# Kernel tuning notes

Hardware: AMD Instinct MI355X
Metric: run time of the kernel (lower is better)

Reference implementation:

```python
import jax, jax.numpy as jnp
import numpy as np

N = 100000      # nodes (single node type)
E = 400000      # edges per relation
R = 4           # relations
DIN = 128       # h_dim
H1 = 8          # heads, layer 1
DH1 = DIN // H1 # per-head dim, layer 1
DOUT = 128      # out_dim (layer 2 has 1 head of dim DOUT)
NEG_SLOPE = 0.2 # GATConv default leaky_relu slope


def gat_rel_layer(h, src, dst, W, al, ar, loop_w, bias, activation):
    """One RelationalAttLayer: per-relation GATConv (bias=False), summed across
    relations, + self-loop matmul + bias + optional relu. dropout=0.
    h: [N, din]; src/dst: [R, E]; W: [R, din, H*Dh]; al/ar: [R, H, Dh];
    loop_w: [din, dout]; bias: [dout]."""
    n = h.shape[0]

    def per_rel(src_r, dst_r, W_r, al_r, ar_r):
        nh, dh = al_r.shape
        Wh = (h @ W_r).reshape(n, nh, dh)                 # [N,H,Dh]
        el = jnp.sum(Wh * al_r, axis=-1)                  # [N,H]
        er = jnp.sum(Wh * ar_r, axis=-1)                  # [N,H]
        e = jax.nn.leaky_relu(el[src_r] + er[dst_r], NEG_SLOPE)  # [E,H]
        # edge-softmax over incoming edges per destination node (stable)
        m = jax.lax.stop_gradient(jax.ops.segment_max(e, dst_r, num_segments=n))
        ex = jnp.exp(e - m[dst_r])
        denom = jax.ops.segment_sum(ex, dst_r, num_segments=n)  # [N,H]
        alpha = ex / denom[dst_r]                                # [E,H]
        # scatter-aggregate messages
        return jax.ops.segment_sum(alpha[:, :, None] * Wh[src_r], dst_r,
                                   num_segments=n)               # [N,H,Dh]

    outs = jax.vmap(per_rel)(src, dst, W, al, ar)  # [R,N,H,Dh]
    hout = outs.sum(0).reshape(n, -1)              # cross-relation sum, flatten heads
    hout = hout + h @ loop_w + bias                # self-loop + h_bias
    if activation:
        hout = jax.nn.relu(hout)
    return hout


def setup_inputs() -> dict:
    key = jax.random.key(0)
    ks = jax.random.split(key, 14)
    s = 0.1
    return {
        "h": jax.random.normal(ks[0], (N, DIN), dtype=jnp.float32),
        "src_idx": jax.random.randint(ks[1], (R, E), 0, N, dtype=jnp.int32),
        "dst_idx": jax.random.randint(ks[2], (R, E), 0, N, dtype=jnp.int32),
        # layer 1 params (h_dim -> h_dim, H1 heads)
        "W1": jax.random.normal(ks[3], (R, DIN, H1 * DH1), dtype=jnp.float32) * s,
        "al1": jax.random.normal(ks[4], (R, H1, DH1), dtype=jnp.float32) * s,
        "ar1": jax.random.normal(ks[5], (R, H1, DH1), dtype=jnp.float32) * s,
        "loop1": jax.random.normal(ks[6], (DIN, DIN), dtype=jnp.float32) * s,
        "b1": jnp.zeros((DIN,), dtype=jnp.float32),
        # layer 2 params (h_dim -> out_dim, 1 head)
        "W2": jax.random.normal(ks[7], (R, DIN, DOUT), dtype=jnp.float32) * s,
        "al2": jax.random.normal(ks[8], (R, 1, DOUT), dtype=jnp.float32) * s,
        "ar2": jax.random.normal(ks[9], (R, 1, DOUT), dtype=jnp.float32) * s,
        "loop2": jax.random.normal(ks[10], (DIN, DOUT), dtype=jnp.float32) * s,
        "b2": jnp.zeros((DOUT,), dtype=jnp.float32),
    }


def reference(h, src_idx, dst_idx, W1, al1, ar1, loop1, b1,
              W2, al2, ar2, loop2, b2):
    # hidden layer: relu activation; last layer: no activation (last_layer_act=False)
    h1 = gat_rel_layer(h, src_idx, dst_idx, W1, al1, ar1, loop1, b1, activation=True)
    h2 = gat_rel_layer(h1, src_idx, dst_idx, W2, al2, ar2, loop2, b2, activation=False)
    return h2
```

## Files before the change

kernel.cpp:

```cpp
#include <hip/hip_runtime.h>

#define NN 100000
#define NE 400000
#define NREL 4
#define MAXDEG 24

typedef unsigned short u16;
typedef __attribute__((ext_vector_type(8))) short bf16x8;
typedef __attribute__((ext_vector_type(4))) float f32x4;

__device__ __forceinline__ u16 f2bf(float x) {
    union { float f; unsigned int u; } v; v.f = x;
    unsigned int r = v.u + 0x7fffu + ((v.u >> 16) & 1u);
    return (u16)(r >> 16);
}
__device__ __forceinline__ float bf2f(u16 x) {
    union { unsigned int u; float f; } v; v.u = ((unsigned int)x) << 16;
    return v.f;
}

template <bool RELU>
__global__ __launch_bounds__(256) void conv_kernel(
    const float* __restrict__ X, u16* __restrict__ Xb, int n8)
{
    int i = blockIdx.x * 256 + threadIdx.x;
    if (i >= n8) return;
    float4 a = ((const float4*)X)[2 * i];
    float4 b = ((const float4*)X)[2 * i + 1];
    if (RELU) {
        a.x = fmaxf(a.x, 0.f); a.y = fmaxf(a.y, 0.f);
        a.z = fmaxf(a.z, 0.f); a.w = fmaxf(a.w, 0.f);
        b.x = fmaxf(b.x, 0.f); b.y = fmaxf(b.y, 0.f);
        b.z = fmaxf(b.z, 0.f); b.w = fmaxf(b.w, 0.f);
    }
    ushort4 lo, hi;
    lo.x = f2bf(a.x); lo.y = f2bf(a.y); lo.z = f2bf(a.z); lo.w = f2bf(a.w);
    hi.x = f2bf(b.x); hi.y = f2bf(b.y); hi.z = f2bf(b.z); hi.w = f2bf(b.w);
    ((ushort4*)Xb)[2 * i] = lo;
    ((ushort4*)Xb)[2 * i + 1] = hi;
}

__global__ __launch_bounds__(256) void build_b_kernel(
    const float* __restrict__ W, const float* __restrict__ loopw,
    u16* __restrict__ Bb)
{
    int id = blockIdx.x * 256 + threadIdx.x;
    if (id >= 5 * 16384) return;
    int j = id >> 14, rem = id & 16383;
    int c = rem >> 7, k = rem & 127;
    const float* M = (j < 4) ? (W + j * 16384) : loopw;
    Bb[id] = f2bf(M[k * 128 + c]);
}

__global__ __launch_bounds__(256) void build_w_kernel(
    const float* __restrict__ W, const float* __restrict__ al,
    const float* __restrict__ ar, u16* __restrict__ wcatB, int nh, int dh)
{
    int id = blockIdx.x * 256 + threadIdx.x;
    if (id >= 16384) return;
    int j = id >> 7, k = id & 127;
    int P2 = 8 * nh;
    float s = 0.f;
    if (j < P2) {
        int half = 4 * nh;
        int jj = (j < half) ? j : j - half;
        const float* av = (j < half) ? al : ar;
        int r = jj / nh, h = jj % nh;
        for (int i = 0; i < dh; ++i)
            s += W[r * 16384 + k * 128 + h * dh + i] * av[(r * nh + h) * dh + i];
    }
    wcatB[j * 128 + k] = f2bf(s);
}

__global__ __launch_bounds__(256) void csr_build_kernel(
    const int* __restrict__ src, const int* __restrict__ dst,
    int* __restrict__ cur, int* __restrict__ bucket)
{
    int i = blockIdx.x * 256 + threadIdx.x;
    if (i >= NE) return;
    int d0 = dst[i],          s0 = src[i];
    int d1 = dst[NE + i],     s1 = src[NE + i];
    int d2 = dst[2 * NE + i], s2 = src[2 * NE + i];
    int d3 = dst[3 * NE + i], s3 = src[3 * NE + i];
    int p0 = atomicAdd(&cur[d0], 1);
    int p1 = atomicAdd(&cur[NN + d1], 1);
    int p2 = atomicAdd(&cur[2 * NN + d2], 1);
    int p3 = atomicAdd(&cur[3 * NN + d3], 1);
    if (p0 < MAXDEG) bucket[(size_t)d0 * MAXDEG + p0] = s0;
    if (p1 < MAXDEG) bucket[((size_t)NN + d1) * MAXDEG + p1] = s1;
    if (p2 < MAXDEG) bucket[((size_t)2 * NN + d2) * MAXDEG + p2] = s2;
    if (p3 < MAXDEG) bucket[((size_t)3 * NN + d3) * MAXDEG + p3] = s3;
}

__global__ __launch_bounds__(256) void fused_gemm_kernel(
    const u16* __restrict__ Xb, const u16* __restrict__ Bb,
    const u16* __restrict__ wcatB, u16* __restrict__ Wh,
    float* __restrict__ O, const float* __restrict__ bias,
    float* __restrict__ elr, int P2, int n)
{
    __shared__ u16 sA[64][136];
    __shared__ u16 sB[128][136];
    const int tid = threadIdx.x;
    const int y = blockIdx.y;
    const int row0 = blockIdx.x * 64;
    const u16* Bmat = (y < 5) ? (Bb + (size_t)y * 16384) : wcatB;

#pragma unroll
    for (int i = 0; i < 8; ++i) {
        int idx = tid + 256 * i;
        int r = idx >> 4, ch = idx & 15;
        *(float4*)&sB[r][ch * 8] = ((const float4*)Bmat)[idx];
    }
#pragma unroll
    for (int i = 0; i < 4; ++i) {
        int idx = tid + 256 * i;
        int r = idx >> 4, ch = idx & 15;
        int gr = row0 + r;
        float4 v = make_float4(0.f, 0.f, 0.f, 0.f);
        if (gr < n) v = *(const float4*)(Xb + (size_t)gr * 128 + ch * 8);
        *(float4*)&sA[r][ch * 8] = v;
    }
    __syncthreads();

    const int w = tid >> 6, lane = tid & 63;
    const int lr = lane & 15, hi = lane >> 4;
    f32x4 acc[8];
#pragma unroll
    for (int fn = 0; fn < 8; ++fn) acc[fn] = (f32x4){0.f, 0.f, 0.f, 0.f};
#pragma unroll
    for (int ko = 0; ko < 4; ++ko) {
        const int kk = ko * 32 + hi * 8;
        bf16x8 a = *(const bf16x8*)&sA[w * 16 + lr][kk];
#pragma unroll
        for (int fn = 0; fn < 8; ++fn) {
            bf16x8 b = *(const bf16x8*)&sB[fn * 16 + lr][kk];
            acc[fn] = __builtin_amdgcn_mfma_f32_16x16x32_bf16(a, b, acc[fn], 0, 0, 0);
        }
    }

    if (y < 4) {
        u16* Wr = Wh + (size_t)y * NN * 128;
#pragma unroll
        for (int reg = 0; reg < 4; ++reg) {
            int grow = row0 + w * 16 + hi * 4 + reg;
            if (grow >= n) continue;
            u16* crow = Wr + (size_t)grow * 128;
#pragma unroll
            for (int fn = 0; fn < 8; ++fn)
                crow[fn * 16 + lr] = f2bf(acc[fn][reg]);
        }
    } else if (y == 4) {
#pragma unroll
        for (int reg = 0; reg < 4; ++reg) {
            int grow = row0 + w * 16 + hi * 4 + reg;
            if (grow >= n) continue;
            float* crow = O + (size_t)grow * 128;
#pragma unroll
            for (int fn = 0; fn < 8; ++fn) {
                int col = fn * 16 + lr;
                crow[col] = acc[fn][reg] + bias[col];
            }
        }
    } else {
#pragma unroll
        for (int reg = 0; reg < 4; ++reg) {
            int grow = row0 + w * 16 + hi * 4 + reg;
            if (grow >= n) continue;
#pragma unroll
            for (int fn = 0; fn < 8; ++fn) {
                int col = fn * 16 + lr;
                if (col < P2) elr[(size_t)grow * P2 + col] = acc[fn][reg];
            }
        }
    }
}

__global__ __launch_bounds__(256) void gather_kernel(
    const int* __restrict__ cnt, const int* __restrict__ bucket,
    const float* __restrict__ elr, const u16* __restrict__ Wh,
    float* __restrict__ O, int ST, int nh, int dh_shift)
{
    const int d = blockIdx.x;
    const int w = threadIdx.x >> 6;
    const int lane = threadIdx.x & 63;
    const int c0 = lane * 2;
    const int hh = c0 >> dh_shift;
    __shared__ float2 part[4][64];

    float M0 = 0.f, M1 = 0.f;
    int deg = cnt[w * NN + d];
    deg = deg > MAXDEG ? MAXDEG : deg;
    if (deg > 0) {
        const int* bk = bucket + ((size_t)w * NN + d) * MAXDEG;
        const float erd = elr[(size_t)d * ST + NREL * nh + w * nh + hh];
        const u16* whr = Wh + (size_t)w * NN * 128;
        const int eo = w * nh + hh;
        float dn = 0.f, m0 = 0.f, m1 = 0.f;
        int e = 0;
        for (; e + 4 <= deg; e += 4) {
            int4 q = *(const int4*)(bk + e);
            float va = elr[(size_t)q.x * ST + eo];
            float vb = elr[(size_t)q.y * ST + eo];
            float vc = elr[(size_t)q.z * ST + eo];
            float vd = elr[(size_t)q.w * ST + eo];
            ushort2 wa = *(const ushort2*)(whr + (size_t)q.x * 128 + c0);
            ushort2 wb = *(const ushort2*)(whr + (size_t)q.y * 128 + c0);
            ushort2 wc = *(const ushort2*)(whr + (size_t)q.z * 128 + c0);
            ushort2 wd = *(const ushort2*)(whr + (size_t)q.w * 128 + c0);
            float v, ex;
            v = va + erd; v = v > 0.f ? v : 0.2f * v; ex = __expf(v);
            dn += ex; m0 = fmaf(ex, bf2f(wa.x), m0); m1 = fmaf(ex, bf2f(wa.y), m1);
            v = vb + erd; v = v > 0.f ? v : 0.2f * v; ex = __expf(v);
            dn += ex; m0 = fmaf(ex, bf2f(wb.x), m0); m1 = fmaf(ex, bf2f(wb.y), m1);
            v = vc + erd; v = v > 0.f ? v : 0.2f * v; ex = __expf(v);
            dn += ex; m0 = fmaf(ex, bf2f(wc.x), m0); m1 = fmaf(ex, bf2f(wc.y), m1);
            v = vd + erd; v = v > 0.f ? v : 0.2f * v; ex = __expf(v);
            dn += ex; m0 = fmaf(ex, bf2f(wd.x), m0); m1 = fmaf(ex, bf2f(wd.y), m1);
        }
        for (; e < deg; ++e) {
            int s = bk[e];
            float v = elr[(size_t)s * ST + eo] + erd;
            v = v > 0.f ? v : 0.2f * v;
            float ex = __expf(v);
            ushort2 wv = *(const ushort2*)(whr + (size_t)s * 128 + c0);
            dn += ex;
            m0 = fmaf(ex, bf2f(wv.x), m0);
            m1 = fmaf(ex, bf2f(wv.y), m1);
        }
        float inv = 1.f / dn;
        M0 = m0 * inv; M1 = m1 * inv;
    }
    part[w][lane] = make_float2(M0, M1);
    __syncthreads();
    if (w == 0) {
        float2 a = part[0][lane], b = part[1][lane];
        float2 c = part[2][lane], e4 = part[3][lane];
        float2* op = (float2*)(O + (size_t)d * 128) + lane;
        float2 cc = *op;
        cc.x += a.x + b.x + c.x + e4.x;
        cc.y += a.y + b.y + c.y + e4.y;
        *op = cc;
    }
}

static void run_layer(const u16* Xb, float* O, const float* W,
                      const float* al, const float* ar, const float* loopw,
                      const float* biasv, int nh, int dh, int dh_shift,
                      const int* cnt, const int* bucket,
                      u16* Wh, float* elr, u16* Bb, u16* wcatB,
                      hipStream_t stream)
{
    const int P2 = 8 * nh;
    build_b_kernel<<<(5 * 16384) / 256, 256, 0, stream>>>(W, loopw, Bb);
    build_w_kernel<<<16384 / 256, 256, 0, stream>>>(W, al, ar, wcatB, nh, dh);

    const int gg = (NN + 63) / 64;
    fused_gemm_kernel<<<dim3(gg, 6), 256, 0, stream>>>(
        Xb, Bb, wcatB, Wh, O, biasv, elr, P2, NN);
    gather_kernel<<<NN, 256, 0, stream>>>(cnt, bucket, elr, Wh, O, P2, nh, dh_shift);
}

extern "C" void kernel_launch(void* const* d_in, const int* in_sizes, int n_in,
                              void* d_out, int out_size, void* d_ws, size_t ws_size,
                              hipStream_t stream)
{
    const float* h   = (const float*)d_in[0];
    const int*   src = (const int*)d_in[1];
    const int*   dst = (const int*)d_in[2];
    const float* W1  = (const float*)d_in[3];
    const float* al1 = (const float*)d_in[4];
    const float* ar1 = (const float*)d_in[5];
    const float* lp1 = (const float*)d_in[6];
    const float* b1  = (const float*)d_in[7];
    const float* W2  = (const float*)d_in[8];
    const float* al2 = (const float*)d_in[9];
    const float* ar2 = (const float*)d_in[10];
    const float* lp2 = (const float*)d_in[11];
    const float* b2  = (const float*)d_in[12];

    float* out = (float*)d_out;
    char*  p   = (char*)d_ws;

    const size_t szXb  = (size_t)NN * 128 * 2;
    const size_t szO   = (size_t)NN * 128 * 4;
    const size_t szElr = (size_t)NN * 64 * 4;
    const size_t szCnt = (size_t)NREL * NN * 4;
    const size_t szBkt = (size_t)NREL * NN * MAXDEG * 4;
    const size_t szBb  = 5 * 16384 * 2;
    const size_t szWc  = 16384 * 2;

    u16*   Xb     = (u16*)p;    p += szXb;
    float* O1     = (float*)p;  p += szO;
    float* elr    = (float*)p;  p += szElr;
    int*   cnt    = (int*)p;    p += szCnt;
    int*   bucket = (int*)p;    p += szBkt;
    u16*   Bb     = (u16*)p;    p += szBb;
    u16*   wcatB  = (u16*)p;    p += szWc;
    u16*   Wh     = (u16*)p;

    hipMemsetAsync(cnt, 0, szCnt, stream);
    csr_build_kernel<<<(NE + 255) / 256, 256, 0, stream>>>(src, dst, cnt, bucket);

    const int n8 = NN * 128 / 8;
    conv_kernel<false><<<(n8 + 255) / 256, 256, 0, stream>>>(h, Xb, n8);
    run_layer(Xb, O1, W1, al1, ar1, lp1, b1, 8, 16, 4,
              cnt, bucket, Wh, elr, Bb, wcatB, stream);
    conv_kernel<true><<<(n8 + 255) / 256, 256, 0, stream>>>(O1, Xb, n8);
    run_layer(Xb, out, W2, al2, ar2, lp2, b2, 1, 128, 7,
              cnt, bucket, Wh, elr, Bb, wcatB, stream);
}
```

Baseline: 760.1 us.

## Aggregate raw features before projection in layer 2 and split per-relation gathers

Layer 2 has a single head, so the attention-weighted sum of W·x over neighbours equals W applied to the weighted sum of x. The new code first gathers neighbour rows of the bf16 input per relation, then runs one K=640 GEMM that covers the four relation weights and the self-loop weight. This drops the per-relation projected Wh tensor for layer 2. Layer 1 now launches one gather per relation with four destinations per block, so the shared-memory reduction and block sync go away, and the logits are stored in a per-relation layout. The cost is an extra bf16 rounding of the aggregated features and more kernel launches.

```diff
diff --git a/kernel.cpp b/kernel.cpp
--- a/kernel.cpp
+++ b/kernel.cpp
@@ -17,6 +17,12 @@
 __device__ __forceinline__ float bf2f(u16 x) {
     union { unsigned int u; float f; } v; v.u = ((unsigned int)x) << 16;
     return v.f;
+}
+
+__global__ __launch_bounds__(256) void zero_cnt_kernel(int* __restrict__ cnt, int n)
+{
+    int i = blockIdx.x * 256 + threadIdx.x;
+    if (i < n) cnt[i] = 0;
 }
 
 template <bool RELU>
@@ -40,16 +46,16 @@
     ((ushort4*)Xb)[2 * i + 1] = hi;
 }
 
-__global__ __launch_bounds__(256) void build_b_kernel(
+__global__ __launch_bounds__(256) void build_bcat_kernel(
     const float* __restrict__ W, const float* __restrict__ loopw,
-    u16* __restrict__ Bb)
+    u16* __restrict__ Bcat)
 {
     int id = blockIdx.x * 256 + threadIdx.x;
     if (id >= 5 * 16384) return;
-    int j = id >> 14, rem = id & 16383;
+    int slot = id >> 14, rem = id & 16383;
     int c = rem >> 7, k = rem & 127;
-    const float* M = (j < 4) ? (W + j * 16384) : loopw;
-    Bb[id] = f2bf(M[k * 128 + c]);
+    const float* M = (slot < 4) ? (W + slot * 16384) : loopw;
+    Bcat[(size_t)c * 640 + slot * 128 + k] = f2bf(M[k * 128 + c]);
 }
 
 __global__ __launch_bounds__(256) void build_w_kernel(
@@ -65,9 +71,9 @@
         int half = 4 * nh;
         int jj = (j < half) ? j : j - half;
         const float* av = (j < half) ? al : ar;
-        int r = jj / nh, h = jj % nh;
+        int r = jj / nh, hh = jj % nh;
         for (int i = 0; i < dh; ++i)
-            s += W[r * 16384 + k * 128 + h * dh + i] * av[(r * nh + h) * dh + i];
+            s += W[r * 16384 + k * 128 + hh * dh + i] * av[(r * nh + hh) * dh + i];
     }
     wcatB[j * 128 + k] = f2bf(s);
 }
@@ -93,23 +99,25 @@
 }
 
 __global__ __launch_bounds__(256) void fused_gemm_kernel(
-    const u16* __restrict__ Xb, const u16* __restrict__ Bb,
+    const u16* __restrict__ Xb, const u16* __restrict__ Bcat,
     const u16* __restrict__ wcatB, u16* __restrict__ Wh,
     float* __restrict__ O, const float* __restrict__ bias,
-    float* __restrict__ elr, int P2, int n)
+    float* __restrict__ elrR, int n)
 {
     __shared__ u16 sA[64][136];
     __shared__ u16 sB[128][136];
     const int tid = threadIdx.x;
     const int y = blockIdx.y;
     const int row0 = blockIdx.x * 64;
-    const u16* Bmat = (y < 5) ? (Bb + (size_t)y * 16384) : wcatB;
+    const u16* bbase; int bstride;
+    if (y < 5) { bbase = Bcat + y * 128; bstride = 640; }
+    else       { bbase = wcatB;          bstride = 128; }
 
 #pragma unroll
     for (int i = 0; i < 8; ++i) {
         int idx = tid + 256 * i;
         int r = idx >> 4, ch = idx & 15;
-        *(float4*)&sB[r][ch * 8] = ((const float4*)Bmat)[idx];
+        *(float4*)&sB[r][ch * 8] = *(const float4*)(bbase + (size_t)r * bstride + ch * 8);
     }
 #pragma unroll
     for (int i = 0; i < 4; ++i) {
@@ -169,95 +177,227 @@
 #pragma unroll
             for (int fn = 0; fn < 8; ++fn) {
                 int col = fn * 16 + lr;
-                if (col < P2) elr[(size_t)grow * P2 + col] = acc[fn][reg];
+                if (col < 64) {
+                    int jj  = (col < 32) ? col : col - 32;
+                    int r   = jj >> 3, hh = jj & 7;
+                    int off = (col < 32) ? hh : 8 + hh;
+                    elrR[((size_t)r * NN + grow) * 16 + off] = acc[fn][reg];
+                }
             }
         }
     }
 }
 
-__global__ __launch_bounds__(256) void gather_kernel(
+__global__ __launch_bounds__(256) void elr2_gemm_kernel(
+    const u16* __restrict__ Xb, const u16* __restrict__ wcatB,
+    float* __restrict__ elrR, int n)
+{
+    __shared__ u16 sA[64][136];
+    __shared__ u16 sB[16][136];
+    const int tid = threadIdx.x;
+    const int row0 = blockIdx.x * 64;
+
+    if (tid < 256) {
+        int r = tid >> 4, ch = tid & 15;
+        *(float4*)&sB[r][ch * 8] = *(const float4*)(wcatB + (size_t)r * 128 + ch * 8);
+    }
+#pragma unroll
+    for (int i = 0; i < 4; ++i) {
+        int idx = tid + 256 * i;
+        int r = idx >> 4, ch = idx & 15;
+        int gr = row0 + r;
+        float4 v = make_float4(0.f, 0.f, 0.f, 0.f);
+        if (gr < n) v = *(const float4*)(Xb + (size_t)gr * 128 + ch * 8);
+        *(float4*)&sA[r][ch * 8] = v;
+    }
+    __syncthreads();
+
+    const int w = tid >> 6, lane = tid & 63;
+    const int lr = lane & 15, hi = lane >> 4;
+    f32x4 acc = (f32x4){0.f, 0.f, 0.f, 0.f};
+#pragma unroll
+    for (int ko = 0; ko < 4; ++ko) {
+        const int kk = ko * 32 + hi * 8;
+        bf16x8 a = *(const bf16x8*)&sA[w * 16 + lr][kk];
+        bf16x8 b = *(const bf16x8*)&sB[lr][kk];
+        acc = __builtin_amdgcn_mfma_f32_16x16x32_bf16(a, b, acc, 0, 0, 0);
+    }
+#pragma unroll
+    for (int reg = 0; reg < 4; ++reg) {
+        int grow = row0 + w * 16 + hi * 4 + reg;
+        if (grow >= n) continue;
+        int col = lr;
+        if (col < 8) {
+            int r = (col < 4) ? col : col - 4;
+            int off = (col < 4) ? 0 : 1;
+            elrR[((size_t)r * NN + grow) * 2 + off] = acc[reg];
+        }
+    }
+}
+
+__global__ __launch_bounds__(256) void gather_rel_kernel(
     const int* __restrict__ cnt, const int* __restrict__ bucket,
-    const float* __restrict__ elr, const u16* __restrict__ Wh,
-    float* __restrict__ O, int ST, int nh, int dh_shift)
+    const float* __restrict__ elP, const u16* __restrict__ WhR,
+    float* __restrict__ O)
+{
+    const int d = blockIdx.x * 4 + (threadIdx.x >> 6);
+    if (d >= NN) return;
+    const int lane = threadIdx.x & 63;
+    const int c0 = lane * 2;
+    const int hh = c0 >> 4;
+
+    int deg = cnt[d];
+    deg = deg < 0 ? 0 : (deg > MAXDEG ? MAXDEG : deg);
+    const int* bk = bucket + (size_t)d * MAXDEG;
+    int4 q0 = make_int4(0, 0, 0, 0), q1 = make_int4(0, 0, 0, 0);
+    if (deg > 0) q0 = *(const int4*)bk;
+    if (deg > 4) q1 = *(const int4*)(bk + 4);
+    const float erd = elP[(size_t)d * 16 + 8 + hh];
+
+    float dn = 0.f, m0 = 0.f, m1 = 0.f;
+    const int ss[8] = {q0.x, q0.y, q0.z, q0.w, q1.x, q1.y, q1.z, q1.w};
+#pragma unroll
+    for (int e = 0; e < 8; ++e) {
+        int s = ss[e];
+        s = ((unsigned)s < (unsigned)NN) ? s : 0;
+        float v = elP[(size_t)s * 16 + hh] + erd;
+        ushort2 wv = *(const ushort2*)(WhR + (size_t)s * 128 + c0);
+        v = v > 0.f ? v : 0.2f * v;
+        float ex = (e < deg) ? __expf(v) : 0.f;
+        dn += ex;
+        m0 = fmaf(ex, bf2f(wv.x), m0);
+        m1 = fmaf(ex, bf2f(wv.y), m1);
+    }
+    for (int e = 8; e < deg; ++e) {
+        int s = bk[e];
+        s = ((unsigned)s < (unsigned)NN) ? s : 0;
+        float v = elP[(size_t)s * 16 + hh] + erd;
+        v = v > 0.f ? v : 0.2f * v;
+        float ex = __expf(v);
+        ushort2 wv = *(const ushort2*)(WhR + (size_t)s * 128 + c0);
+        dn += ex;
+        m0 = fmaf(ex, bf2f(wv.x), m0);
+        m1 = fmaf(ex, bf2f(wv.y), m1);
+    }
+    float inv = (deg > 0) ? 1.f / dn : 0.f;
+    float2* op = (float2*)(O + (size_t)d * 128) + lane;
+    float2 c = *op;
+    c.x += m0 * inv;
+    c.y += m1 * inv;
+    *op = c;
+}
+
+__global__ __launch_bounds__(256) void gather_x_kernel(
+    const int* __restrict__ cnt, const int* __restrict__ bucket,
+    const float* __restrict__ elrR, const u16* __restrict__ Xb,
+    u16* __restrict__ Xagg)
 {
     const int d = blockIdx.x;
     const int w = threadIdx.x >> 6;
     const int lane = threadIdx.x & 63;
     const int c0 = lane * 2;
-    const int hh = c0 >> dh_shift;
-    __shared__ float2 part[4][64];
-
-    float M0 = 0.f, M1 = 0.f;
+
     int deg = cnt[w * NN + d];
-    deg = deg > MAXDEG ? MAXDEG : deg;
-    if (deg > 0) {
-        const int* bk = bucket + ((size_t)w * NN + d) * MAXDEG;
-        const float erd = elr[(size_t)d * ST + NREL * nh + w * nh + hh];
-        const u16* whr = Wh + (size_t)w * NN * 128;
-        const int eo = w * nh + hh;
-        float dn = 0.f, m0 = 0.f, m1 = 0.f;
-        int e = 0;
-        for (; e + 4 <= deg; e += 4) {
-            int4 q = *(const int4*)(bk + e);
-            float va = elr[(size_t)q.x * ST + eo];
-            float vb = elr[(size_t)q.y * ST + eo];
-            float vc = elr[(size_t)q.z * ST + eo];
-            float vd = elr[(size_t)q.w * ST + eo];
-            ushort2 wa = *(const ushort2*)(whr + (size_t)q.x * 128 + c0);
-            ushort2 wb = *(const ushort2*)(whr + (size_t)q.y * 128 + c0);
-            ushort2 wc = *(const ushort2*)(whr + (size_t)q.z * 128 + c0);
-            ushort2 wd = *(const ushort2*)(whr + (size_t)q.w * 128 + c0);
-            float v, ex;
-            v = va + erd; v = v > 0.f ? v : 0.2f * v; ex = __expf(v);
-            dn += ex; m0 = fmaf(ex, bf2f(wa.x), m0); m1 = fmaf(ex, bf2f(wa.y), m1);
-            v = vb + erd; v = v > 0.f ? v : 0.2f * v; ex = __expf(v);
-            dn += ex; m0 = fmaf(ex, bf2f(wb.x), m0); m1 = fmaf(ex, bf2f(wb.y), m1);
-            v = vc + erd; v = v > 0.f ? v : 0.2f * v; ex = __expf(v);
-            dn += ex; m0 = fmaf(ex, bf2f(wc.x), m0); m1 = fmaf(ex, bf2f(wc.y), m1);
-            v = vd + erd; v = v > 0.f ? v : 0.2f * v; ex = __expf(v);
-            dn += ex; m0 = fmaf(ex, bf2f(wd.x), m0); m1 = fmaf(ex, bf2f(wd.y), m1);
-        }
-        for (; e < deg; ++e) {
-            int s = bk[e];
-            float v = elr[(size_t)s * ST + eo] + erd;
-            v = v > 0.f ? v : 0.2f * v;
-            float ex = __expf(v);
-            ushort2 wv = *(const ushort2*)(whr + (size_t)s * 128 + c0);
-            dn += ex;
-            m0 = fmaf(ex, bf2f(wv.x), m0);
-            m1 = fmaf(ex, bf2f(wv.y), m1);
-        }
-        float inv = 1.f / dn;
-        M0 = m0 * inv; M1 = m1 * inv;
-    }
-    part[w][lane] = make_float2(M0, M1);
-    __syncthreads();
-    if (w == 0) {
-        float2 a = part[0][lane], b = part[1][lane];
-        float2 c = part[2][lane], e4 = part[3][lane];
-        float2* op = (float2*)(O + (size_t)d * 128) + lane;
-        float2 cc = *op;
-        cc.x += a.x + b.x + c.x + e4.x;
-        cc.y += a.y + b.y + c.y + e4.y;
-        *op = cc;
-    }
-}
-
-static void run_layer(const u16* Xb, float* O, const float* W,
-                      const float* al, const float* ar, const float* loopw,
-                      const float* biasv, int nh, int dh, int dh_shift,
-                      const int* cnt, const int* bucket,
-                      u16* Wh, float* elr, u16* Bb, u16* wcatB,
-                      hipStream_t stream)
-{
-    const int P2 = 8 * nh;
-    build_b_kernel<<<(5 * 16384) / 256, 256, 0, stream>>>(W, loopw, Bb);
-    build_w_kernel<<<16384 / 256, 256, 0, stream>>>(W, al, ar, wcatB, nh, dh);
-
-    const int gg = (NN + 63) / 64;
-    fused_gemm_kernel<<<dim3(gg, 6), 256, 0, stream>>>(
-        Xb, Bb, wcatB, Wh, O, biasv, elr, P2, NN);
-    gather_kernel<<<NN, 256, 0, stream>>>(cnt, bucket, elr, Wh, O, P2, nh, dh_shift);
+    deg = deg < 0 ? 0 : (deg > MAXDEG ? MAXDEG : deg);
+    const int* bk = bucket + ((size_t)w * NN + d) * MAXDEG;
+    int4 q0 = make_int4(0, 0, 0, 0), q1 = make_int4(0, 0, 0, 0);
+    if (deg > 0) q0 = *(const int4*)bk;
+    if (deg > 4) q1 = *(const int4*)(bk + 4);
+    const float* elP = elrR + (size_t)w * NN * 2;
+    const float erd = elP[(size_t)d * 2 + 1];
+
+    float dn = 0.f, m0 = 0.f, m1 = 0.f;
+    const int ss[8] = {q0.x, q0.y, q0.z, q0.w, q1.x, q1.y, q1.z, q1.w};
+#pragma unroll
+    for (int e = 0; e < 8; ++e) {
+        int s = ss[e];
+        s = ((unsigned)s < (unsigned)NN) ? s : 0;
+        float v = elP[(size_t)s * 2] + erd;
+        ushort2 wv = *(const ushort2*)(Xb + (size_t)s * 128 + c0);
+        v = v > 0.f ? v : 0.2f * v;
+        float ex = (e < deg) ? __expf(v) : 0.f;
+        dn += ex;
+        m0 = fmaf(ex, bf2f(wv.x), m0);
+        m1 = fmaf(ex, bf2f(wv.y), m1);
+    }
+    for (int e = 8; e < deg; ++e) {
+        int s = bk[e];
+        s = ((unsigned)s < (unsigned)NN) ? s : 0;
+        float v = elP[(size_t)s * 2] + erd;
+        v = v > 0.f ? v : 0.2f * v;
+        float ex = __expf(v);
+        ushort2 wv = *(const ushort2*)(Xb + (size_t)s * 128 + c0);
+        dn += ex;
+        m0 = fmaf(ex, bf2f(wv.x), m0);
+        m1 = fmaf(ex, bf2f(wv.y), m1);
+    }
+    float inv = (deg > 0) ? 1.f / dn : 0.f;
+    u16* orow = Xagg + ((size_t)w * NN + d) * 128;
+    ushort2 o;
+    o.x = f2bf(m0 * inv);
+    o.y = f2bf(m1 * inv);
+    *(ushort2*)(orow + c0) = o;
+}
+
+__global__ __launch_bounds__(256) void big_gemm_kernel(
+    const u16* __restrict__ Xagg, const u16* __restrict__ Xb,
+    const u16* __restrict__ Bcat, const float* __restrict__ bias,
+    float* __restrict__ out, int n)
+{
+    __shared__ u16 sA[64][136];
+    __shared__ u16 sB[128][136];
+    const int tid = threadIdx.x;
+    const int row0 = blockIdx.x * 64;
+    const int w = tid >> 6, lane = tid & 63;
+    const int lr = lane & 15, hi = lane >> 4;
+
+    f32x4 acc[8];
+#pragma unroll
+    for (int fn = 0; fn < 8; ++fn) acc[fn] = (f32x4){0.f, 0.f, 0.f, 0.f};
+
+    for (int kc = 0; kc < 5; ++kc) {
+        const u16* Amat = (kc < 4) ? (Xagg + (size_t)kc * NN * 128) : Xb;
+        if (kc) __syncthreads();
+#pragma unroll
+        for (int i = 0; i < 8; ++i) {
+            int idx = tid + 256 * i;
+            int r = idx >> 4, ch = idx & 15;
+            *(float4*)&sB[r][ch * 8] =
+                *(const float4*)(Bcat + (size_t)r * 640 + kc * 128 + ch * 8);
+        }
+#pragma unroll
+        for (int i = 0; i < 4; ++i) {
+            int idx = tid + 256 * i;
+            int r = idx >> 4, ch = idx & 15;
+            int gr = row0 + r;
+            float4 v = make_float4(0.f, 0.f, 0.f, 0.f);
+            if (gr < n) v = *(const float4*)(Amat + (size_t)gr * 128 + ch * 8);
+            *(float4*)&sA[r][ch * 8] = v;
+        }
+        __syncthreads();
+#pragma unroll
+        for (int ko = 0; ko < 4; ++ko) {
+            const int kk = ko * 32 + hi * 8;
+            bf16x8 a = *(const bf16x8*)&sA[w * 16 + lr][kk];
+#pragma unroll
+            for (int fn = 0; fn < 8; ++fn) {
+                bf16x8 b = *(const bf16x8*)&sB[fn * 16 + lr][kk];
+                acc[fn] = __builtin_amdgcn_mfma_f32_16x16x32_bf16(a, b, acc[fn], 0, 0, 0);
+            }
+        }
+    }
+
+#pragma unroll
+    for (int reg = 0; reg < 4; ++reg) {
+        int grow = row0 + w * 16 + hi * 4 + reg;
+        if (grow >= n) continue;
+        float* crow = out + (size_t)grow * 128;
+#pragma unroll
+        for (int fn = 0; fn < 8; ++fn) {
+            int col = fn * 16 + lr;
+            crow[col] = acc[fn][reg] + bias[col];
+        }
+    }
 }
 
 extern "C" void kernel_launch(void* const* d_in, const int* in_sizes, int n_in,
@@ -281,31 +421,43 @@
     float* out = (float*)d_out;
     char*  p   = (char*)d_ws;
 
-    const size_t szXb  = (size_t)NN * 128 * 2;
-    const size_t szO   = (size_t)NN * 128 * 4;
-    const size_t szElr = (size_t)NN * 64 * 4;
-    const size_t szCnt = (size_t)NREL * NN * 4;
-    const size_t szBkt = (size_t)NREL * NN * MAXDEG * 4;
-    const size_t szBb  = 5 * 16384 * 2;
-    const size_t szWc  = 16384 * 2;
+    const size_t szXb   = (size_t)NN * 128 * 2;
+    const size_t szO    = (size_t)NN * 128 * 4;
+    const size_t szElr  = (size_t)NREL * NN * 16 * 4;
+    const size_t szCnt  = (size_t)NREL * NN * 4;
+    const size_t szBkt  = (size_t)NREL * NN * MAXDEG * 4;
+    const size_t szBcat = 5 * 16384 * 2;
+    const size_t szWc   = 16384 * 2;
 
     u16*   Xb     = (u16*)p;    p += szXb;
     float* O1     = (float*)p;  p += szO;
-    float* elr    = (float*)p;  p += szElr;
+    float* elrR   = (float*)p;  p += szElr;
     int*   cnt    = (int*)p;    p += szCnt;
     int*   bucket = (int*)p;    p += szBkt;
-    u16*   Bb     = (u16*)p;    p += szBb;
+    u16*   Bcat   = (u16*)p;    p += szBcat;
     u16*   wcatB  = (u16*)p;    p += szWc;
     u16*   Wh     = (u16*)p;
 
-    hipMemsetAsync(cnt, 0, szCnt, stream);
+    const int gg = (NN + 63) / 64;
+    const int n8 = NN * 128 / 8;
+
+    zero_cnt_kernel<<<(NREL * NN + 255) / 256, 256, 0, stream>>>(cnt, NREL * NN);
     csr_build_kernel<<<(NE + 255) / 256, 256, 0, stream>>>(src, dst, cnt, bucket);
-
-    const int n8 = NN * 128 / 8;
     conv_kernel<false><<<(n8 + 255) / 256, 256, 0, stream>>>(h, Xb, n8);
-    run_layer(Xb, O1, W1, al1, ar1, lp1, b1, 8, 16, 4,
-              cnt, bucket, Wh, elr, Bb, wcatB, stream);
+
+    build_bcat_kernel<<<(5 * 16384) / 256, 256, 0, stream>>>(W1, lp1, Bcat);
+    build_w_kernel<<<16384 / 256, 256, 0, stream>>>(W1, al1, ar1, wcatB, 8, 16);
+    fused_gemm_kernel<<<dim3(gg, 6), 256, 0, stream>>>(
+        Xb, Bcat, wcatB, Wh, O1, b1, elrR, NN);
+    for (int r = 0; r < NREL; ++r)
+        gather_rel_kernel<<<(NN + 3) / 4, 256, 0, stream>>>(
+            cnt + (size_t)r * NN, bucket + (size_t)r * NN * MAXDEG,
+            elrR + (size_t)r * NN * 16, Wh + (size_t)r * NN * 128, O1);
     conv_kernel<true><<<(n8 + 255) / 256, 256, 0, stream>>>(O1, Xb, n8);
-    run_layer(Xb, out, W2, al2, ar2, lp2, b2, 1, 128, 7,
-              cnt, bucket, Wh, elr, Bb, wcatB, stream);
-}
+
+    build_bcat_kernel<<<(5 * 16384) / 256, 256, 0, stream>>>(W2, lp2, Bcat);
+    build_w_kernel<<<16384 / 256, 256, 0, stream>>>(W2, al2, ar2, wcatB, 1, 128);
+    elr2_gemm_kernel<<<gg, 256, 0, stream>>>(Xb, wcatB, elrR, NN);
+    gather_x_kernel<<<NN, 256, 0, stream>>>(cnt, bucket, elrR, Xb, Wh);
+    big_gemm_kernel<<<gg, 256, 0, stream>>>(Wh, Xb, Bcat, b2, out, NN);
+}
```

New measurement: 789.7 us. 1.04x slower.
